# Performance work log

Hardware: AMD Instinct MI355X
Metric: run time of the kernel (lower is better)

## Reference

```python
import jax, jax.numpy as jnp
import numpy as np

INPUT_DIM = 256
OUTPUT_DIM = 256
COND_DIM = 128
HIDDEN = 128
BATCH = 512


def setup_inputs() -> dict:
    key = jax.random.key(0)
    ks = jax.random.split(key, 8)
    IO = INPUT_DIM * OUTPUT_DIM
    x = jax.random.normal(ks[0], (BATCH, INPUT_DIM), dtype=jnp.float32)
    cond = jax.random.normal(ks[1], (BATCH, COND_DIM), dtype=jnp.float32)
    base_weight = jax.random.normal(ks[2], (INPUT_DIM, OUTPUT_DIM), dtype=jnp.float32) * 0.01
    base_bias = jnp.zeros((OUTPUT_DIM,), dtype=jnp.float32)
    # hypernet: Linear(cond_dim, hidden) -> ReLU -> Linear(hidden, I*O + O)
    w1 = jax.random.normal(ks[3], (COND_DIM, HIDDEN), dtype=jnp.float32) * (1.0 / np.sqrt(COND_DIM))
    b1 = jnp.zeros((HIDDEN,), dtype=jnp.float32)
    w2 = jax.random.normal(ks[4], (HIDDEN, IO + OUTPUT_DIM), dtype=jnp.float32) * (1.0 / np.sqrt(HIDDEN))
    b2 = jnp.zeros((IO + OUTPUT_DIM,), dtype=jnp.float32)
    return {"x": x, "cond": cond, "base_weight": base_weight, "base_bias": base_bias,
            "w1": w1, "b1": b1, "w2": w2, "b2": b2}


def reference(x, cond, base_weight, base_bias, w1, b1, w2, b2):
    B = x.shape[0]
    IO = INPUT_DIM * OUTPUT_DIM
    # hypernet MLP producing per-sample weight/bias deltas
    h = jax.nn.relu(cond @ w1 + b1)                      # [B, hidden]
    dyn = h @ w2 + b2                                    # [B, I*O + O]
    weight_delta = dyn[:, :IO].reshape(B, INPUT_DIM, OUTPUT_DIM)
    bias_delta = dyn[:, IO:]                             # [B, O]
    W = base_weight[None, :, :] + weight_delta           # [B, I, O]
    b = base_bias[None, :] + bias_delta                  # [B, O]
    out = jnp.einsum('bi,bio->bo', x, W) + b             # per-sample GEMV
    return out
```

## Files before the change

kernel.cpp:

```cpp
#include <hip/hip_runtime.h>
#include <hip/hip_bf16.h>
#include <stdint.h>

#define BATCH    512
#define IN_DIM   256
#define OUT_DIM  256
#define COND_DIM 128
#define HIDDEN   128
#define W2_COLS  65792
#define H_STRIDE 132
#define PLANE_SZ 65536
#define NCHUNKS  34
#define OUT_ELEMS (BATCH * OUT_DIM)
#define SLICE_OFF ((size_t)131 * PLANE_SZ)

typedef __attribute__((ext_vector_type(8))) short bf16x8;
typedef __attribute__((ext_vector_type(4))) float f32x4;

__device__ float          g_h[BATCH * H_STRIDE + 8];
__device__ unsigned short g_hbf[BATCH * HIDDEN];
__device__ unsigned short g_xbf[BATCH * IN_DIM];

static __device__ __forceinline__ unsigned short f2bf(float f) {
    union { float f; unsigned int u; } v; v.f = f;
    unsigned int r = v.u + 0x7FFFu + ((v.u >> 16) & 1u);
    return (unsigned short)(r >> 16);
}
static __device__ __forceinline__ unsigned int pack2(float a, float b) {
    return (unsigned int)f2bf(a) | ((unsigned int)f2bf(b) << 16);
}
static __device__ __forceinline__ float bf2f(unsigned short u) {
    union { unsigned int u; float f; } v; v.u = ((unsigned int)u) << 16;
    return v.f;
}

__global__ __launch_bounds__(256)
void hyper_prep_kernel(const float* __restrict__ x,
                       const float* __restrict__ cond,
                       const float* __restrict__ base_weight,
                       const float* __restrict__ w1,
                       const float* __restrict__ b1,
                       const float* __restrict__ w2,
                       const float* __restrict__ b2,
                       unsigned short* __restrict__ wt) {
    const int bx = blockIdx.x;
    const int t  = threadIdx.x;
    if (bx < 2088) {
        int p, it, ot; const float* src; int rstride;
        if (bx < 2080) {
            p = bx >> 4; int sub = bx & 15; it = sub >> 2; ot = sub & 3;
            src = (p < 128) ? (w2 + (size_t)p * W2_COLS) : (p == 128 ? b2 : base_weight);
            rstride = OUT_DIM;
        } else {
            p = 130; int sub = bx - 2080; it = sub >> 2; ot = sub & 3;
            src = w2 + 65536; rstride = W2_COLS;
        }
        int o  = ot * 64 + (t & 63);
        int i0 = it * 64 + (t >> 6) * 16;
        unsigned int vv[8];
        #pragma unroll
        for (int r = 0; r < 8; ++r) {
            float a = src[(size_t)(i0 + 2 * r)     * rstride + o];
            float b = src[(size_t)(i0 + 2 * r + 1) * rstride + o];
            vv[r] = pack2(a, b);
        }
        unsigned int* dst = (unsigned int*)(wt + (size_t)p * PLANE_SZ + (size_t)o * 256 + i0);
        *(uint4*)dst       = *(uint4*)&vv[0];
        *(uint4*)(dst + 4) = *(uint4*)&vv[4];
    } else if (bx < 2104) {
        int base = (bx - 2088) * 8192 + t * 32;
        #pragma unroll
        for (int g = 0; g < 4; ++g) {
            const float4* s4 = (const float4*)(x + base + g * 8);
            float4 a = s4[0], b = s4[1];
            unsigned int vv[4] = { pack2(a.x, a.y), pack2(a.z, a.w),
                                   pack2(b.x, b.y), pack2(b.z, b.w) };
            *(uint4*)(g_xbf + base + g * 8) = *(uint4*)vv;
        }
    } else {
        __shared__ float c[2][COND_DIM];
        int bb = t >> 7, k = t & 127;
        int b  = (bx - 2104) * 2 + bb;
        c[bb][k] = cond[b * COND_DIM + k];
        __syncthreads();
        float acc = b1[k];
        #pragma unroll 8
        for (int i = 0; i < COND_DIM; ++i)
            acc += c[bb][i] * w1[i * HIDDEN + k];
        acc = fmaxf(acc, 0.0f);
        g_h[b * H_STRIDE + k] = acc;
        g_hbf[b * HIDDEN + k] = f2bf(acc);
        if (k < 4) g_h[b * H_STRIDE + 128 + k] = 1.0f;
    }
}

template<int NSLABS>
static __device__ __forceinline__ void run_gemm(
    int nplanes, int p0, const unsigned short* asrc, int astride,
    const unsigned short* __restrict__ wt, unsigned short* __restrict__ slices,
    int chunk, int b0, int o0, int t,
    unsigned short (*B_lds)[64 * 64], float* h_s)
{
    const int lane = t & 63, wave = t >> 6;
    const int wm = wave >> 1, wn = wave & 1;
    const int qg = lane >> 4, ncol = lane & 15;

    const int drow = lane >> 3;
    const int dcol = ((lane & 7) ^ drow) * 8;

    bf16x8 xf[NSLABS][2][2];
    #pragma unroll
    for (int sl = 0; sl < NSLABS; ++sl)
        #pragma unroll
        for (int ks = 0; ks < 2; ++ks)
            #pragma unroll
            for (int mf = 0; mf < 2; ++mf)
                xf[sl][ks][mf] = *(const bf16x8*)(asrc
                    + (size_t)(b0 + wm * 32 + mf * 16 + ncol) * astride
                    + sl * 64 + ks * 32 + qg * 8);

    f32x4 acc[2][2] = {};
    f32x4 pacc[2][2];
    float hv[2][4];

    auto dmaB = [&](int plane, int i0, int buf) {
        const unsigned short* gp = wt + (size_t)plane * PLANE_SZ
            + (size_t)(o0 + wave * 16 + drow) * 256 + i0 + dcol;
        __builtin_amdgcn_global_load_lds(
            (const __attribute__((address_space(1))) unsigned int*)gp,
            (__attribute__((address_space(3))) unsigned int*)&B_lds[buf][wave * 16 * 64],
            16, 0, 0);
        __builtin_amdgcn_global_load_lds(
            (const __attribute__((address_space(1))) unsigned int*)(gp + 8 * 256),
            (__attribute__((address_space(3))) unsigned int*)&B_lds[buf][(wave * 16 + 8) * 64],
            16, 0, 0);
    };

    dmaB(p0, 0, 0);
    __syncthreads();

    for (int pl = 0; pl < nplanes; ++pl) {
        #pragma unroll
        for (int sl = 0; sl < NSLABS; ++sl) {
            const int buf = sl & 1;
            if (sl + 1 < NSLABS)          dmaB(p0 + pl,     (sl + 1) * 64, buf ^ 1);
            else if (pl + 1 < nplanes)    dmaB(p0 + pl + 1, 0,             buf ^ 1);

            if (sl == 0) {
                #pragma unroll
                for (int mf = 0; mf < 2; ++mf)
                    #pragma unroll
                    for (int r = 0; r < 4; ++r)
                        hv[mf][r] = h_s[(wm * 32 + mf * 16 + qg * 4 + r) * 4 + pl];
                #pragma unroll
                for (int a = 0; a < 2; ++a)
                    #pragma unroll
                    for (int bq = 0; bq < 2; ++bq)
                        pacc[a][bq] = (f32x4){0.f, 0.f, 0.f, 0.f};
            }

            #pragma unroll
            for (int ks = 0; ks < 2; ++ks) {
                bf16x8 bfr[2];
                #pragma unroll
                for (int nf = 0; nf < 2; ++nf) {
                    int n = wn * 32 + nf * 16 + ncol;
                    bfr[nf] = *(const bf16x8*)&B_lds[buf][(n * 8 + ((ks * 4 + qg) ^ (n & 7))) * 8];
                }
                #pragma unroll
                for (int mf = 0; mf < 2; ++mf)
                    #pragma unroll
                    for (int nf = 0; nf < 2; ++nf)
                        pacc[mf][nf] = __builtin_amdgcn_mfma_f32_16x16x32_bf16(
                            xf[sl][ks][mf], bfr[nf], pacc[mf][nf], 0, 0, 0);
            }

            if (sl == NSLABS - 1) {
                #pragma unroll
                for (int mf = 0; mf < 2; ++mf)
                    #pragma unroll
                    for (int nf = 0; nf < 2; ++nf)
                        #pragma unroll
                        for (int r = 0; r < 4; ++r)
                            acc[mf][nf][r] += hv[mf][r] * pacc[mf][nf][r];
            }
            __syncthreads();
        }
    }

    unsigned short* slice = slices + (size_t)chunk * OUT_ELEMS;
    #pragma unroll
    for (int mf = 0; mf < 2; ++mf)
        #pragma unroll
        for (int nf = 0; nf < 2; ++nf)
            #pragma unroll
            for (int r = 0; r < 4; ++r) {
                int row = b0 + wm * 32 + mf * 16 + qg * 4 + r;
                int col = o0 + wn * 32 + nf * 16 + ncol;
                slice[(size_t)row * OUT_DIM + col] = f2bf(acc[mf][nf][r]);
            }
}

__global__ __launch_bounds__(256, 3)
void hyper_main_kernel(const unsigned short* __restrict__ wt,
                       unsigned short* __restrict__ slices) {
    __shared__ __align__(16) unsigned short B_lds[2][64 * 64];
    __shared__ float h_s[256];

    const int bx    = blockIdx.x;
    const int chunk = bx >> 5;
    const int rem   = bx & 31;
    const int b0    = (rem >> 2) * 64;
    const int o0    = (rem & 3) * 64;
    const int t     = threadIdx.x;

    int p0 = (chunk < 32) ? chunk * 4 : (chunk == 32 ? 128 : 130);

    h_s[t] = g_h[(b0 + (t >> 2)) * H_STRIDE + p0 + (t & 3)];

    if (chunk < 33)
        run_gemm<4>(chunk < 32 ? 4 : 2, p0, g_xbf, IN_DIM,
                    wt, slices, chunk, b0, o0, t, B_lds, h_s);
    else
        run_gemm<2>(1, p0, g_hbf, HIDDEN,
                    wt, slices, chunk, b0, o0, t, B_lds, h_s);
}

__global__ void hyper_reduce_kernel(const unsigned short* __restrict__ slices,
                                    const float* __restrict__ base_bias,
                                    const float* __restrict__ b2,
                                    float* __restrict__ out) {
    int i = blockIdx.x * 256 + threadIdx.x;
    int o = (i & 63) * 4;
    float4 bb = *(const float4*)(base_bias + o);
    float4 c2 = *(const float4*)(b2 + 65536 + o);
    float4 a;
    a.x = bb.x + c2.x; a.y = bb.y + c2.y; a.z = bb.z + c2.z; a.w = bb.w + c2.w;
    #pragma unroll
    for (int c = 0; c < NCHUNKS; ++c) {
        ushort4 v = *(const ushort4*)(slices + (size_t)c * OUT_ELEMS + (size_t)i * 4);
        a.x += bf2f(v.x); a.y += bf2f(v.y); a.z += bf2f(v.z); a.w += bf2f(v.w);
    }
    ((float4*)out)[i] = a;
}

extern "C" void kernel_launch(void* const* d_in, const int* in_sizes, int n_in,
                              void* d_out, int out_size, void* d_ws, size_t ws_size,
                              hipStream_t stream) {
    const float* x           = (const float*)d_in[0];
    const float* cond        = (const float*)d_in[1];
    const float* base_weight = (const float*)d_in[2];
    const float* base_bias   = (const float*)d_in[3];
    const float* w1          = (const float*)d_in[4];
    const float* b1          = (const float*)d_in[5];
    const float* w2          = (const float*)d_in[6];
    const float* b2          = (const float*)d_in[7];
    float* out = (float*)d_out;
    unsigned short* ws = (unsigned short*)d_ws;

    hyper_prep_kernel<<<2360, 256, 0, stream>>>(x, cond, base_weight, w1, b1, w2, b2, ws);
    hyper_main_kernel<<<NCHUNKS * 32, 256, 0, stream>>>(ws, ws + SLICE_OFF);
    hyper_reduce_kernel<<<OUT_ELEMS / 4 / 256, 256, 0, stream>>>(ws + SLICE_OFF, base_bias, b2, out);
}
```

Baseline: 123.8 us.

## Stage activations in LDS and stream weight planes directly into registers

The GEMM no longer double-buffers the weight tiles in LDS through global_load_lds with a barrier after every slab. Instead the activation tile (x or h in bf16) is staged once into swizzled LDS. Each wave then loads its B fragments directly from global memory into registers, and the plane/slab counts become compile-time template parameters. This removes per-slab __syncthreads and LDS round trips for the large weight stream. In exchange, global loads are exposed per wave without explicit prefetch, so it relies on occupancy and the compiler to hide latency.

New measurement: 142.3 us. 1.15x slower.

```diff
diff --git a/kernel.cpp b/kernel.cpp
--- a/kernel.cpp
+++ b/kernel.cpp
@@ -94,98 +94,80 @@
     }
 }
 
-template<int NSLABS>
+template<int NPL, int NSL>
 static __device__ __forceinline__ void run_gemm(
-    int nplanes, int p0, const unsigned short* asrc, int astride,
+    int p0, const unsigned short* __restrict__ asrc,
     const unsigned short* __restrict__ wt, unsigned short* __restrict__ slices,
     int chunk, int b0, int o0, int t,
-    unsigned short (*B_lds)[64 * 64], float* h_s)
+    unsigned short* __restrict__ A_lds, const float* __restrict__ h_s)
 {
+    constexpr int UNITS = NSL * 8;
     const int lane = t & 63, wave = t >> 6;
     const int wm = wave >> 1, wn = wave & 1;
     const int qg = lane >> 4, ncol = lane & 15;
-
-    const int drow = lane >> 3;
-    const int dcol = ((lane & 7) ^ drow) * 8;
-
-    bf16x8 xf[NSLABS][2][2];
+    const int sw = ncol & 7;
+
+    {
+        const int r = t >> 2, nu = UNITS / 4, u0 = (t & 3) * nu;
+        const unsigned short* srow = asrc + (size_t)(b0 + r) * (UNITS * 8) + u0 * 8;
+        #pragma unroll
+        for (int q = 0; q < nu; ++q) {
+            uint4 v = *(const uint4*)(srow + q * 8);
+            *(uint4*)&A_lds[((size_t)r * UNITS + ((u0 + q) ^ (r & 7))) * 8] = v;
+        }
+    }
+    __syncthreads();
+
+    const unsigned short* bbase = wt + (size_t)p0 * PLANE_SZ
+        + (size_t)(o0 + wn * 32 + ncol) * 256 + qg * 8;
+
+    f32x4 acc[2][2] = {};
+
     #pragma unroll
-    for (int sl = 0; sl < NSLABS; ++sl)
-        #pragma unroll
-        for (int ks = 0; ks < 2; ++ks)
-            #pragma unroll
-            for (int mf = 0; mf < 2; ++mf)
-                xf[sl][ks][mf] = *(const bf16x8*)(asrc
-                    + (size_t)(b0 + wm * 32 + mf * 16 + ncol) * astride
-                    + sl * 64 + ks * 32 + qg * 8);
-
-    f32x4 acc[2][2] = {};
-    f32x4 pacc[2][2];
-    float hv[2][4];
-
-    auto dmaB = [&](int plane, int i0, int buf) {
-        const unsigned short* gp = wt + (size_t)plane * PLANE_SZ
-            + (size_t)(o0 + wave * 16 + drow) * 256 + i0 + dcol;
-        __builtin_amdgcn_global_load_lds(
-            (const __attribute__((address_space(1))) unsigned int*)gp,
-            (__attribute__((address_space(3))) unsigned int*)&B_lds[buf][wave * 16 * 64],
-            16, 0, 0);
-        __builtin_amdgcn_global_load_lds(
-            (const __attribute__((address_space(1))) unsigned int*)(gp + 8 * 256),
-            (__attribute__((address_space(3))) unsigned int*)&B_lds[buf][(wave * 16 + 8) * 64],
-            16, 0, 0);
-    };
-
-    dmaB(p0, 0, 0);
-    __syncthreads();
-
-    for (int pl = 0; pl < nplanes; ++pl) {
-        #pragma unroll
-        for (int sl = 0; sl < NSLABS; ++sl) {
-            const int buf = sl & 1;
-            if (sl + 1 < NSLABS)          dmaB(p0 + pl,     (sl + 1) * 64, buf ^ 1);
-            else if (pl + 1 < nplanes)    dmaB(p0 + pl + 1, 0,             buf ^ 1);
-
-            if (sl == 0) {
+    for (int pl = 0; pl < NPL; ++pl) {
+        f32x4 pacc[2][2];
+        float hv[2][4];
+        #pragma unroll
+        for (int mf = 0; mf < 2; ++mf)
+            #pragma unroll
+            for (int r = 0; r < 4; ++r)
+                hv[mf][r] = h_s[(wm * 32 + mf * 16 + qg * 4 + r) * 4 + pl];
+
+        #pragma unroll
+        for (int sl = 0; sl < NSL; ++sl) {
+            bf16x8 bfr[2][2], af[2][2];
+            #pragma unroll
+            for (int ks = 0; ks < 2; ++ks) {
+                #pragma unroll
+                for (int nf = 0; nf < 2; ++nf)
+                    bfr[ks][nf] = *(const bf16x8*)(bbase + (size_t)pl * PLANE_SZ
+                        + sl * 64 + ks * 32 + nf * 16 * 256);
+                #pragma unroll
+                for (int mf = 0; mf < 2; ++mf) {
+                    int m = wm * 32 + mf * 16 + ncol;
+                    af[ks][mf] = *(const bf16x8*)&A_lds[
+                        ((size_t)m * UNITS + ((sl * 8 + ks * 4 + qg) ^ sw)) * 8];
+                }
+            }
+            #pragma unroll
+            for (int ks = 0; ks < 2; ++ks)
                 #pragma unroll
                 for (int mf = 0; mf < 2; ++mf)
                     #pragma unroll
-                    for (int r = 0; r < 4; ++r)
-                        hv[mf][r] = h_s[(wm * 32 + mf * 16 + qg * 4 + r) * 4 + pl];
-                #pragma unroll
-                for (int a = 0; a < 2; ++a)
-                    #pragma unroll
-                    for (int bq = 0; bq < 2; ++bq)
-                        pacc[a][bq] = (f32x4){0.f, 0.f, 0.f, 0.f};
-            }
-
-            #pragma unroll
-            for (int ks = 0; ks < 2; ++ks) {
-                bf16x8 bfr[2];
-                #pragma unroll
-                for (int nf = 0; nf < 2; ++nf) {
-                    int n = wn * 32 + nf * 16 + ncol;
-                    bfr[nf] = *(const bf16x8*)&B_lds[buf][(n * 8 + ((ks * 4 + qg) ^ (n & 7))) * 8];
-                }
-                #pragma unroll
-                for (int mf = 0; mf < 2; ++mf)
-                    #pragma unroll
-                    for (int nf = 0; nf < 2; ++nf)
+                    for (int nf = 0; nf < 2; ++nf) {
+                        f32x4 c = (sl == 0 && ks == 0) ? (f32x4){0.f, 0.f, 0.f, 0.f}
+                                                       : pacc[mf][nf];
                         pacc[mf][nf] = __builtin_amdgcn_mfma_f32_16x16x32_bf16(
-                            xf[sl][ks][mf], bfr[nf], pacc[mf][nf], 0, 0, 0);
-            }
-
-            if (sl == NSLABS - 1) {
-                #pragma unroll
-                for (int mf = 0; mf < 2; ++mf)
-                    #pragma unroll
-                    for (int nf = 0; nf < 2; ++nf)
-                        #pragma unroll
-                        for (int r = 0; r < 4; ++r)
-                            acc[mf][nf][r] += hv[mf][r] * pacc[mf][nf][r];
-            }
-            __syncthreads();
-        }
+                            af[ks][mf], bfr[ks][nf], c, 0, 0, 0);
+                    }
+        }
+        #pragma unroll
+        for (int mf = 0; mf < 2; ++mf)
+            #pragma unroll
+            for (int nf = 0; nf < 2; ++nf)
+                #pragma unroll
+                for (int r = 0; r < 4; ++r)
+                    acc[mf][nf][r] += hv[mf][r] * pacc[mf][nf][r];
     }
 
     unsigned short* slice = slices + (size_t)chunk * OUT_ELEMS;
@@ -204,7 +186,7 @@
 __global__ __launch_bounds__(256, 3)
 void hyper_main_kernel(const unsigned short* __restrict__ wt,
                        unsigned short* __restrict__ slices) {
-    __shared__ __align__(16) unsigned short B_lds[2][64 * 64];
+    __shared__ __align__(16) unsigned short A_lds[64 * 32 * 8];
     __shared__ float h_s[256];
 
     const int bx    = blockIdx.x;
@@ -214,16 +196,16 @@
     const int o0    = (rem & 3) * 64;
     const int t     = threadIdx.x;
 
-    int p0 = (chunk < 32) ? chunk * 4 : (chunk == 32 ? 128 : 130);
+    const int p0 = (chunk < 32) ? chunk * 4 : (chunk == 32 ? 128 : 130);
 
     h_s[t] = g_h[(b0 + (t >> 2)) * H_STRIDE + p0 + (t & 3)];
 
-    if (chunk < 33)
-        run_gemm<4>(chunk < 32 ? 4 : 2, p0, g_xbf, IN_DIM,
-                    wt, slices, chunk, b0, o0, t, B_lds, h_s);
+    if (chunk < 32)
+        run_gemm<4, 4>(p0, g_xbf, wt, slices, chunk, b0, o0, t, A_lds, h_s);
+    else if (chunk == 32)
+        run_gemm<2, 4>(p0, g_xbf, wt, slices, chunk, b0, o0, t, A_lds, h_s);
     else
-        run_gemm<2>(1, p0, g_hbf, HIDDEN,
-                    wt, slices, chunk, b0, o0, t, B_lds, h_s);
+        run_gemm<1, 2>(p0, g_hbf, wt, slices, chunk, b0, o0, t, A_lds, h_s);
 }
 
 __global__ void hyper_reduce_kernel(const unsigned short* __restrict__ slices,
```
